# Performance work log

Hardware: AMD Instinct MI355X
Metric: run time of the kernel (lower is better)

Reference implementation:

```python
import jax, jax.numpy as jnp
import numpy as np

B, L, D, M = 8, 4096, 512, 64


def setup_inputs() -> dict:
    key = jax.random.key(0)
    k1, k2, k3 = jax.random.split(key, 3)
    scale = 1.0 / (D * D)
    return {
        "q": jax.random.normal(k1, (B, L, D), dtype=jnp.float32),
        "w_real": scale * jax.random.normal(k2, (D, D, M), dtype=jnp.float32),
        "w_imag": scale * jax.random.normal(k3, (D, D, M), dtype=jnp.float32),
    }


def reference(q, w_real, w_imag):
    # q: [B, L, D]; weights: [D, D, modes]
    b, l, d = q.shape
    n_freq = l // 2 + 1
    q_ft = jnp.fft.rfft(q, axis=1)                      # [B, n_freq, D] complex64
    m = min(w_real.shape[-1], n_freq)
    W = w_real[..., :m] + 1j * w_imag[..., :m]          # [D, E, m] complex
    # Batched over modes: replaces the per-mode python loop with one einsum.
    out_m = jnp.einsum('bmd,dem->bme', q_ft[:, :m, :], W)  # [B, m, D]
    out_ft = jnp.zeros((b, n_freq, d), dtype=q_ft.dtype).at[:, :m, :].set(out_m)
    return jnp.fft.irfft(out_ft, n=l, axis=1)           # [B, L, D] float32
```

## Files before the change

kernel.cpp:

```cpp
#include <hip/hip_runtime.h>

#define B_ 8
#define L_ 4096
#define D_ 512
#define M_ 64

typedef __attribute__((ext_vector_type(8))) short bh8;
typedef __attribute__((ext_vector_type(4))) float f4;
typedef __attribute__((ext_vector_type(4))) unsigned u32x4;

__device__ inline unsigned short f2bf(float f) {
  unsigned u = __float_as_uint(f);
  return (unsigned short)((u + 0x7fffu + ((u >> 16) & 1u)) >> 16);
}
__device__ inline unsigned packbf(float lo, float hi) {
  return (unsigned)f2bf(lo) | ((unsigned)f2bf(hi) << 16);
}

__global__ void k_ftab(unsigned short* __restrict__ F) {
  int t = blockIdx.x * 256 + threadIdx.x;
  int r = t >> 12, l = t & 4095;
  int k = r & 63, part = r >> 6;
  int ph = (k * l) & (L_ - 1);
  double ang = 6.283185307179586476925286766559 * (double)ph / (double)L_;
  float v = part ? (float)(-sin(ang)) : (float)(cos(ang));
  F[t] = f2bf(v);
}

__global__ void k_gtab(unsigned short* __restrict__ G) {
  int t = blockIdx.x * 256 + threadIdx.x;
  int l = t >> 7, j = t & 127;
  int k = j & 63, part = j >> 6;
  int ph = (k * l) & (L_ - 1);
  double ang = 6.283185307179586476925286766559 * (double)ph / (double)L_;
  double ck = (k == 0 ? 1.0 : 2.0) / (double)L_;
  float v = part ? (float)(-ck * sin(ang)) : (float)(ck * cos(ang));
  G[t] = f2bf(v);
}

__global__ __launch_bounds__(512, 4) void k_dft_mfma(
    const float* __restrict__ q, const unsigned short* __restrict__ F,
    float* __restrict__ pQ) {
  int tid = threadIdx.x;
  int dt = blockIdx.x, b = blockIdx.y, kc = blockIdx.z;
  int d0 = dt * 64;
  int lbase = kc * 512;

  int w = tid >> 6, lane = tid & 63;
  int mh = w & 3, nc = w >> 2;
  int lr = lane & 15, kg = lane >> 4;

  f4 acc[2][2];
#pragma unroll
  for (int i = 0; i < 2; ++i)
#pragma unroll
    for (int j = 0; j < 2; ++j) { f4 z = {0.f, 0.f, 0.f, 0.f}; acc[i][j] = z; }

  const unsigned short* A0 = F + (size_t)(mh * 32 + lr) * 4096 + lbase + kg * 8;
  const unsigned short* A1 = A0 + (size_t)16 * 4096;
  const float* q0 = q + ((size_t)b * L_ + lbase + kg * 8) * D_ + d0 + nc * 32 + lr;

#pragma unroll 2
  for (int s = 0; s < 16; ++s) {
    const float* qs = q0 + (size_t)s * 32 * D_;
    float v0[8], v1[8];
#pragma unroll
    for (int j = 0; j < 8; ++j) {
      v0[j] = qs[(size_t)j * D_];
      v1[j] = qs[(size_t)j * D_ + 16];
    }
    union { u32x4 u; bh8 h; } bf0, bf1;
    bf0.u.x = packbf(v0[0], v0[1]); bf0.u.y = packbf(v0[2], v0[3]);
    bf0.u.z = packbf(v0[4], v0[5]); bf0.u.w = packbf(v0[6], v0[7]);
    bf1.u.x = packbf(v1[0], v1[1]); bf1.u.y = packbf(v1[2], v1[3]);
    bf1.u.z = packbf(v1[4], v1[5]); bf1.u.w = packbf(v1[6], v1[7]);
    bh8 af0 = *(const bh8*)(A0 + s * 32);
    bh8 af1 = *(const bh8*)(A1 + s * 32);
    acc[0][0] = __builtin_amdgcn_mfma_f32_16x16x32_bf16(af0, bf0.h, acc[0][0], 0, 0, 0);
    acc[0][1] = __builtin_amdgcn_mfma_f32_16x16x32_bf16(af0, bf1.h, acc[0][1], 0, 0, 0);
    acc[1][0] = __builtin_amdgcn_mfma_f32_16x16x32_bf16(af1, bf0.h, acc[1][0], 0, 0, 0);
    acc[1][1] = __builtin_amdgcn_mfma_f32_16x16x32_bf16(af1, bf1.h, acc[1][1], 0, 0, 0);
  }

#pragma unroll
  for (int mi = 0; mi < 2; ++mi) {
    int r = mh * 32 + mi * 16 + kg * 4;
#pragma unroll
    for (int ni = 0; ni < 2; ++ni) {
      int d = d0 + nc * 32 + ni * 16 + lr;
#pragma unroll
      for (int j = 0; j < 4; ++j)
        pQ[(((size_t)kc * 128 + (r + j)) * 8 + b) * 512 + d] = acc[mi][ni][j];
    }
  }
}

__global__ __launch_bounds__(256) void k_red2(const float* __restrict__ pQ,
                                              unsigned* __restrict__ Qbf) {
  int g = blockIdx.x * 256 + threadIdx.x;
  int dq = g & 127;
  int b = (g >> 7) & 7;
  int k = g >> 10;
  f4 sr = {0.f, 0.f, 0.f, 0.f}, si = {0.f, 0.f, 0.f, 0.f};
#pragma unroll
  for (int kc = 0; kc < 8; ++kc) {
    size_t base = (((size_t)kc * 128 + k) * 8 + b) * 512 + dq * 4;
    sr += *(const f4*)(pQ + base);
    si += *(const f4*)(pQ + base + (size_t)64 * 8 * 512);
  }
  u32x4 o;
  o.x = packbf(sr[0], si[0]); o.y = packbf(sr[1], si[1]);
  o.z = packbf(sr[2], si[2]); o.w = packbf(sr[3], si[3]);
  *(u32x4*)(Qbf + ((size_t)k * 8 + b) * 512 + dq * 4) = o;
}

__global__ __launch_bounds__(512, 4) void k_mix_mfma(
    const float* __restrict__ wr_, const float* __restrict__ wi_,
    const unsigned* __restrict__ Qbf, float* __restrict__ pOut) {
  __shared__ unsigned Wt[16384];
  int tid = threadIdx.x;
  int et = blockIdx.x, dc = blockIdx.y;
  int e0 = et * 16;
  int w = tid >> 6, lane = tid & 63;
  int er = lane & 15, kg = lane >> 4;
  int part = er >> 3, b = er & 7;

  f4 acc[8];
#pragma unroll
  for (int t = 0; t < 8; ++t) { f4 z = {0.f, 0.f, 0.f, 0.f}; acc[t] = z; }

  for (int r = 0; r < 4; ++r) {
    if (r) __syncthreads();
    int dbase = dc * 64 + r * 16;
#pragma unroll
    for (int i = 0; i < 8; ++i) {
      int f = tid + i * 512;
      int d_loc = f >> 8;
      int e = (f >> 4) & 15;
      int k4 = f & 15;
      size_t gidx = ((size_t)(dbase + d_loc) * 512 + (e0 + e)) * 16 + k4;
      float4 a  = ((const float4*)wr_)[gidx];
      float4 bb = ((const float4*)wi_)[gidx];
      int dp = d_loc ^ ((k4 & 3) << 2);
      int base = k4 * 1024 + e * 16 + dp;
      Wt[base]       = packbf(a.x, bb.x);
      Wt[base + 256] = packbf(a.y, bb.y);
      Wt[base + 512] = packbf(a.z, bb.z);
      Wt[base + 768] = packbf(a.w, bb.w);
    }
    __syncthreads();
    int d0 = dbase + kg * 4;
#pragma unroll
    for (int t = 0; t < 8; ++t) {
      int k = w * 8 + t;
      int sw = ((k >> 2) & 3) << 2;
      union { u32x4 u; bh8 h; } av, bv;
      av.u = *(const u32x4*)&Wt[k * 256 + er * 16 + ((kg * 4) ^ sw)];
      u32x4 qv = *(const u32x4*)(Qbf + ((size_t)k * 8 + b) * 512 + d0);
      if (part == 0) {
        bv.u.x = qv.x ^ 0x80000000u; bv.u.y = qv.y ^ 0x80000000u;
        bv.u.z = qv.z ^ 0x80000000u; bv.u.w = qv.w ^ 0x80000000u;
      } else {
        bv.u.x = (qv.x >> 16) | (qv.x << 16); bv.u.y = (qv.y >> 16) | (qv.y << 16);
        bv.u.z = (qv.z >> 16) | (qv.z << 16); bv.u.w = (qv.w >> 16) | (qv.w << 16);
      }
      acc[t] = __builtin_amdgcn_mfma_f32_16x16x32_bf16(av.h, bv.h, acc[t], 0, 0, 0);
    }
  }

#pragma unroll
  for (int t = 0; t < 8; ++t) {
    int k = w * 8 + t;
    size_t off = (size_t)dc * 524288 +
                 (((size_t)k * 2 + part) * 8 + b) * 512 + e0 + kg * 4;
    *(f4*)(pOut + off) = acc[t];
  }
}

__global__ __launch_bounds__(256) void k_psum2(const float* __restrict__ pOut,
                                               unsigned* __restrict__ Pw) {
  __shared__ float sP[128 * 33];
  int tid = threadIdx.x;
  int e0 = blockIdx.x * 32, b = blockIdx.y;
  {
    int e = tid & 31, kg4 = tid >> 5;
#pragma unroll
    for (int ii = 0; ii < 16; ++ii) {
      int col = kg4 * 16 + ii;
      int rkp = ((col & 63) << 1) | (col >> 6);
      float s = 0.f;
#pragma unroll
      for (int c = 0; c < 8; ++c)
        s += pOut[(size_t)c * 524288 + (size_t)rkp * 4096 + b * 512 + e0 + e];
      sP[col * 33 + e] = s;
    }
  }
  __syncthreads();
  {
    int e = tid >> 3, c = tid & 7;
    size_t wbase = (((size_t)b * 512 + e0 + e) * 128 + c * 16) >> 1;
#pragma unroll
    for (int ii = 0; ii < 8; ++ii) {
      int col = c * 16 + ii * 2;
      Pw[wbase + ii] = packbf(sP[col * 33 + e], sP[(col + 1) * 33 + e]);
    }
  }
}

#define LST 72
__global__ __launch_bounds__(256, 2) void k_inv_mfma(
    const short* __restrict__ G, const short* __restrict__ P,
    float* __restrict__ y) {
  __shared__ short lds[2 * 128 * LST];
  short* As = lds;
  short* Bs = lds + 128 * LST;

  int tid = threadIdx.x;
  int lt = blockIdx.x, et = blockIdx.y, b = blockIdx.z;
  int l0 = lt * 128, e0 = et * 128;

  int wv = tid >> 6, lane = tid & 63;
  int wrow = wv >> 1, wcol = wv & 1;
  int lr = lane & 15, kg = lane >> 4;

  const short* Gb = G + (size_t)l0 * 128;
  const short* Pb = P + (size_t)b * D_ * 128 + (size_t)e0 * 128;

  f4 acc[4][4];
#pragma unroll
  for (int mi = 0; mi < 4; ++mi)
#pragma unroll
    for (int ni = 0; ni < 4; ++ni) {
      f4 z = {0.f, 0.f, 0.f, 0.f};
      acc[mi][ni] = z;
    }

#pragma unroll
  for (int kh = 0; kh < 2; ++kh) {
    if (kh) __syncthreads();
#pragma unroll
    for (int i = 0; i < 4; ++i) {
      int idx = i * 256 + tid;
      int row = idx >> 3, c = idx & 7;
      *(uint4*)(As + row * LST + c * 8) =
          *(const uint4*)(Gb + (size_t)row * 128 + kh * 64 + c * 8);
      *(uint4*)(Bs + row * LST + c * 8) =
          *(const uint4*)(Pb + (size_t)row * 128 + kh * 64 + c * 8);
    }
    __syncthreads();

#pragma unroll
    for (int ks = 0; ks < 2; ++ks) {
      bh8 a[4], bf[4];
#pragma unroll
      for (int i = 0; i < 4; ++i) {
        a[i]  = *(const bh8*)(As + (wrow * 64 + i * 16 + lr) * LST + ks * 32 + kg * 8);
        bf[i] = *(const bh8*)(Bs + (wcol * 64 + i * 16 + lr) * LST + ks * 32 + kg * 8);
      }
#pragma unroll
      for (int mi = 0; mi < 4; ++mi)
#pragma unroll
        for (int ni = 0; ni < 4; ++ni)
          acc[mi][ni] = __builtin_amdgcn_mfma_f32_16x16x32_bf16(
              a[mi], bf[ni], acc[mi][ni], 0, 0, 0);
    }
  }

#pragma unroll
  for (int mi = 0; mi < 4; ++mi) {
    int lg = l0 + wrow * 64 + mi * 16 + kg * 4;
#pragma unroll
    for (int ni = 0; ni < 4; ++ni) {
      int e = e0 + wcol * 64 + ni * 16 + lr;
#pragma unroll
      for (int j = 0; j < 4; ++j)
        y[((size_t)b * L_ + (lg + j)) * D_ + e] = acc[mi][ni][j];
    }
  }
}

extern "C" void kernel_launch(void* const* d_in, const int* in_sizes, int n_in,
                              void* d_out, int out_size, void* d_ws, size_t ws_size,
                              hipStream_t stream) {
  const float* q  = (const float*)d_in[0];
  const float* wr = (const float*)d_in[1];
  const float* wi = (const float*)d_in[2];
  float* out = (float*)d_out;
  char* ws = (char*)d_ws;

  unsigned short* Fbf = (unsigned short*)ws;
  unsigned short* Gbf = (unsigned short*)(ws + (1u << 20));
  unsigned* Qbf       = (unsigned*)(ws + (2u << 20));
  unsigned* Pw        = (unsigned*)(ws + (3u << 20));

  float* pQ   = out;
  float* pOut = out;

  hipLaunchKernelGGL(k_ftab, dim3((128 * L_) / 256), dim3(256), 0, stream, Fbf);
  hipLaunchKernelGGL(k_gtab, dim3((L_ * 128) / 256), dim3(256), 0, stream, Gbf);
  hipLaunchKernelGGL(k_dft_mfma, dim3(8, 8, 8), dim3(512), 0, stream,
                     q, Fbf, pQ);
  hipLaunchKernelGGL(k_red2, dim3(65536 / 256), dim3(256), 0, stream, pQ, Qbf);
  hipLaunchKernelGGL(k_mix_mfma, dim3(D_ / 16, 8), dim3(512), 0, stream,
                     wr, wi, Qbf, pOut);
  hipLaunchKernelGGL(k_psum2, dim3(16, 8), dim3(256), 0, stream, pOut, Pw);
  hipLaunchKernelGGL(k_inv_mfma, dim3(L_ / 128, D_ / 128, B_), dim3(256), 0,
                     stream, (const short*)Gbf, (const short*)Pw, out);
}
```

Baseline: 107.7 us.

## Pre-pack weights to mode-major bf16 and fuse mode mixing without split-D reduction

Adds a weight-packing kernel that converts the real and imaginary fp32 weights into a mode-major packed bf16 layout in scratch (the output buffer). A new mixing kernel then gives each block one mode and a slice of output channels, and each wave accumulates over the full input dimension. The result is written directly as bf16 in the layout the inverse transform expects. This removes the split-D fp32 partial-sum writes and the separate partial-sum reduction kernel. The cost is an extra full pass writing and re-reading the packed weights, plus strided scalar loads of weights in the mix kernel.

```diff
diff --git a/kernel.cpp b/kernel.cpp
--- a/kernel.cpp
+++ b/kernel.cpp
@@ -114,96 +114,66 @@
   *(u32x4*)(Qbf + ((size_t)k * 8 + b) * 512 + dq * 4) = o;
 }
 
-__global__ __launch_bounds__(512, 4) void k_mix_mfma(
+__global__ __launch_bounds__(256, 8) void k_wpack(
     const float* __restrict__ wr_, const float* __restrict__ wi_,
-    const unsigned* __restrict__ Qbf, float* __restrict__ pOut) {
-  __shared__ unsigned Wt[16384];
+    unsigned* __restrict__ Wp) {
+  const float4* r4 = (const float4*)wr_;
+  const float4* i4 = (const float4*)wi_;
+  int f0 = blockIdx.x * 256 + threadIdx.x;
+#pragma unroll 2
+  for (int it = 0; it < 8; ++it) {
+    int f = f0 + it * 524288;
+    float4 r = r4[f];
+    float4 i = i4[f];
+    int d = f >> 13;
+    int e = (f >> 4) & 511;
+    int k4 = f & 15;
+    unsigned* o = Wp + (size_t)(k4 * 4) * 262144 + d * 512 + e;
+    o[0]      = packbf(r.x, i.x);
+    o[262144] = packbf(r.y, i.y);
+    o[524288] = packbf(r.z, i.z);
+    o[786432] = packbf(r.w, i.w);
+  }
+}
+
+__global__ __launch_bounds__(256, 4) void k_mix2(
+    const unsigned* __restrict__ Wp, const unsigned* __restrict__ Qbf,
+    unsigned short* __restrict__ P) {
   int tid = threadIdx.x;
-  int et = blockIdx.x, dc = blockIdx.y;
-  int e0 = et * 16;
+  int k = blockIdx.x;
+  int et = blockIdx.y;
   int w = tid >> 6, lane = tid & 63;
   int er = lane & 15, kg = lane >> 4;
   int part = er >> 3, b = er & 7;
-
-  f4 acc[8];
-#pragma unroll
-  for (int t = 0; t < 8; ++t) { f4 z = {0.f, 0.f, 0.f, 0.f}; acc[t] = z; }
-
-  for (int r = 0; r < 4; ++r) {
-    if (r) __syncthreads();
-    int dbase = dc * 64 + r * 16;
-#pragma unroll
-    for (int i = 0; i < 8; ++i) {
-      int f = tid + i * 512;
-      int d_loc = f >> 8;
-      int e = (f >> 4) & 15;
-      int k4 = f & 15;
-      size_t gidx = ((size_t)(dbase + d_loc) * 512 + (e0 + e)) * 16 + k4;
-      float4 a  = ((const float4*)wr_)[gidx];
-      float4 bb = ((const float4*)wi_)[gidx];
-      int dp = d_loc ^ ((k4 & 3) << 2);
-      int base = k4 * 1024 + e * 16 + dp;
-      Wt[base]       = packbf(a.x, bb.x);
-      Wt[base + 256] = packbf(a.y, bb.y);
-      Wt[base + 512] = packbf(a.z, bb.z);
-      Wt[base + 768] = packbf(a.w, bb.w);
-    }
-    __syncthreads();
-    int d0 = dbase + kg * 4;
-#pragma unroll
-    for (int t = 0; t < 8; ++t) {
-      int k = w * 8 + t;
-      int sw = ((k >> 2) & 3) << 2;
-      union { u32x4 u; bh8 h; } av, bv;
-      av.u = *(const u32x4*)&Wt[k * 256 + er * 16 + ((kg * 4) ^ sw)];
-      u32x4 qv = *(const u32x4*)(Qbf + ((size_t)k * 8 + b) * 512 + d0);
-      if (part == 0) {
-        bv.u.x = qv.x ^ 0x80000000u; bv.u.y = qv.y ^ 0x80000000u;
-        bv.u.z = qv.z ^ 0x80000000u; bv.u.w = qv.w ^ 0x80000000u;
-      } else {
-        bv.u.x = (qv.x >> 16) | (qv.x << 16); bv.u.y = (qv.y >> 16) | (qv.y << 16);
-        bv.u.z = (qv.z >> 16) | (qv.z << 16); bv.u.w = (qv.w >> 16) | (qv.w << 16);
-      }
-      acc[t] = __builtin_amdgcn_mfma_f32_16x16x32_bf16(av.h, bv.h, acc[t], 0, 0, 0);
-    }
-  }
-
-#pragma unroll
-  for (int t = 0; t < 8; ++t) {
-    int k = w * 8 + t;
-    size_t off = (size_t)dc * 524288 +
-                 (((size_t)k * 2 + part) * 8 + b) * 512 + e0 + kg * 4;
-    *(f4*)(pOut + off) = acc[t];
-  }
-}
-
-__global__ __launch_bounds__(256) void k_psum2(const float* __restrict__ pOut,
-                                               unsigned* __restrict__ Pw) {
-  __shared__ float sP[128 * 33];
-  int tid = threadIdx.x;
-  int e0 = blockIdx.x * 32, b = blockIdx.y;
-  {
-    int e = tid & 31, kg4 = tid >> 5;
-#pragma unroll
-    for (int ii = 0; ii < 16; ++ii) {
-      int col = kg4 * 16 + ii;
-      int rkp = ((col & 63) << 1) | (col >> 6);
-      float s = 0.f;
-#pragma unroll
-      for (int c = 0; c < 8; ++c)
-        s += pOut[(size_t)c * 524288 + (size_t)rkp * 4096 + b * 512 + e0 + e];
-      sP[col * 33 + e] = s;
-    }
-  }
-  __syncthreads();
-  {
-    int e = tid >> 3, c = tid & 7;
-    size_t wbase = (((size_t)b * 512 + e0 + e) * 128 + c * 16) >> 1;
-#pragma unroll
-    for (int ii = 0; ii < 8; ++ii) {
-      int col = c * 16 + ii * 2;
-      Pw[wbase + ii] = packbf(sP[col * 33 + e], sP[(col + 1) * 33 + e]);
-    }
+  int e0 = et * 64 + w * 16;
+
+  const unsigned* wp = Wp + (size_t)k * 262144 + e0 + er;
+  const unsigned* qb = Qbf + ((size_t)k * 8 + b) * 512 + kg * 4;
+
+  f4 acc = {0.f, 0.f, 0.f, 0.f};
+#pragma unroll 4
+  for (int s = 0; s < 32; ++s) {
+    int d = s * 16 + kg * 4;
+    union { u32x4 u; bh8 h; } av, bv;
+    av.u.x = wp[(size_t)(d + 0) * 512];
+    av.u.y = wp[(size_t)(d + 1) * 512];
+    av.u.z = wp[(size_t)(d + 2) * 512];
+    av.u.w = wp[(size_t)(d + 3) * 512];
+    u32x4 q = *(const u32x4*)(qb + s * 16);
+    if (part == 0) {
+      bv.u.x = q.x ^ 0x80000000u; bv.u.y = q.y ^ 0x80000000u;
+      bv.u.z = q.z ^ 0x80000000u; bv.u.w = q.w ^ 0x80000000u;
+    } else {
+      bv.u.x = (q.x >> 16) | (q.x << 16); bv.u.y = (q.y >> 16) | (q.y << 16);
+      bv.u.z = (q.z >> 16) | (q.z << 16); bv.u.w = (q.w >> 16) | (q.w << 16);
+    }
+    acc = __builtin_amdgcn_mfma_f32_16x16x32_bf16(av.h, bv.h, acc, 0, 0, 0);
+  }
+
+#pragma unroll
+  for (int j = 0; j < 4; ++j) {
+    int e = e0 + kg * 4 + j;
+    P[((size_t)b * 512 + e) * 128 + part * 64 + k] = f2bf(acc[j]);
   }
 }
 
@@ -291,19 +261,18 @@
   unsigned short* Fbf = (unsigned short*)ws;
   unsigned short* Gbf = (unsigned short*)(ws + (1u << 20));
   unsigned* Qbf       = (unsigned*)(ws + (2u << 20));
-  unsigned* Pw        = (unsigned*)(ws + (3u << 20));
-
-  float* pQ   = out;
-  float* pOut = out;
+  unsigned short* Pw  = (unsigned short*)(ws + (3u << 20));
+
+  float* pQ    = out;
+  unsigned* Wp = (unsigned*)out;
 
   hipLaunchKernelGGL(k_ftab, dim3((128 * L_) / 256), dim3(256), 0, stream, Fbf);
   hipLaunchKernelGGL(k_gtab, dim3((L_ * 128) / 256), dim3(256), 0, stream, Gbf);
   hipLaunchKernelGGL(k_dft_mfma, dim3(8, 8, 8), dim3(512), 0, stream,
                      q, Fbf, pQ);
   hipLaunchKernelGGL(k_red2, dim3(65536 / 256), dim3(256), 0, stream, pQ, Qbf);
-  hipLaunchKernelGGL(k_mix_mfma, dim3(D_ / 16, 8), dim3(512), 0, stream,
-                     wr, wi, Qbf, pOut);
-  hipLaunchKernelGGL(k_psum2, dim3(16, 8), dim3(256), 0, stream, pOut, Pw);
+  hipLaunchKernelGGL(k_wpack, dim3(2048), dim3(256), 0, stream, wr, wi, Wp);
+  hipLaunchKernelGGL(k_mix2, dim3(64, 8), dim3(256), 0, stream, Wp, Qbf, Pw);
   hipLaunchKernelGGL(k_inv_mfma, dim3(L_ / 128, D_ / 128, B_), dim3(256), 0,
                      stream, (const short*)Gbf, (const short*)Pw, out);
 }
```

After: 146.7 us. +36.2%, slower.
